# Kernel optimization log

Measured on AMD Instinct MI355X. Metric: run time of the kernel, lower is better.

Reference implementation:

```python
import jax, jax.numpy as jnp
import numpy as np
import itertools

DIM = 384
KEY_DIM = 32
NUM_HEADS = 8
ATTN_RATIO = 4
RESOLUTION = 7
D = ATTN_RATIO * KEY_DIM          # 128
DH = D * NUM_HEADS                # 1024
H_QKV = DH + 2 * KEY_DIM * NUM_HEADS  # 1536
B = 2048
N = RESOLUTION ** 2               # 49


def _build_bias_idxs():
    points = list(itertools.product(range(RESOLUTION), range(RESOLUTION)))
    attention_offsets = {}
    idxs = []
    for p1 in points:
        for p2 in points:
            offset = (abs(p1[0] - p2[0]), abs(p1[1] - p2[1]))
            if offset not in attention_offsets:
                attention_offsets[offset] = len(attention_offsets)
            idxs.append(attention_offsets[offset])
    return np.array(idxs, dtype=np.int32).reshape(N, N), len(attention_offsets)


def setup_inputs() -> dict:
    key = jax.random.key(0)
    ks = jax.random.split(key, 6)
    bias_idxs_np, n_offsets = _build_bias_idxs()  # n_offsets == 49 for resolution 7
    x = jax.random.normal(ks[0], (B, N, DIM), dtype=jnp.float32)
    qkv_w = jax.random.normal(ks[1], (H_QKV, DIM), dtype=jnp.float32) * (DIM ** -0.5)
    qkv_b = jnp.zeros((H_QKV,), dtype=jnp.float32)
    proj_w = jax.random.normal(ks[2], (DIM, DH), dtype=jnp.float32) * (DH ** -0.5)
    proj_b = jnp.zeros((DIM,), dtype=jnp.float32)
    attn_bias = jax.random.normal(ks[3], (NUM_HEADS, n_offsets), dtype=jnp.float32) * 0.02
    bias_idxs = jnp.asarray(bias_idxs_np)
    return {"x": x, "qkv_w": qkv_w, "qkv_b": qkv_b, "proj_w": proj_w,
            "proj_b": proj_b, "attn_bias": attn_bias, "bias_idxs": bias_idxs}


def reference(x, qkv_w, qkv_b, proj_w, proj_b, attn_bias, bias_idxs):
    Bb, Nn, _ = x.shape
    scale = KEY_DIM ** -0.5
    qkv = x @ qkv_w.T + qkv_b                       # [B, N, 1536]
    qkv = qkv.reshape(Bb, Nn, NUM_HEADS, KEY_DIM + KEY_DIM + D)
    q = qkv[..., :KEY_DIM]                          # [B, N, H, kd]
    k = qkv[..., KEY_DIM:2 * KEY_DIM]               # [B, N, H, kd]
    v = qkv[..., 2 * KEY_DIM:]                      # [B, N, H, d]
    bias = attn_bias[:, bias_idxs]                  # [H, N, N] gathered rel-pos bias
    attn = jnp.einsum('bnhk,bmhk->bhnm', q, k) * scale + bias
    attn = jax.nn.softmax(attn, axis=-1)
    out = jnp.einsum('bhnm,bmhd->bnhd', attn, v).reshape(Bb, Nn, DH)
    return out @ proj_w.T + proj_b                  # [B, N, dim]
```

## Files before the change

kernel.cpp:

```cpp
#include <hip/hip_runtime.h>
#include <cstddef>
#include <cstdint>

#define TOK    49
#define KD     32
#define NH     8
#define DHEAD  128
#define HQKV   1536
#define DHTOT  1024
#define DIMM   384

typedef unsigned short u16;
typedef float  f32x4  __attribute__((ext_vector_type(4)));
typedef __bf16 bf16x8 __attribute__((ext_vector_type(8)));

typedef const __attribute__((address_space(1))) void gas_void;
typedef __attribute__((address_space(3))) void las_void;

static __device__ __forceinline__ u16 f2bf(float f) {
    unsigned int u = __builtin_bit_cast(unsigned int, f);
    return (u16)((u + 0x7fffu + ((u >> 16) & 1u)) >> 16);
}

static __device__ __forceinline__ int swz(int row, int c) {
    return (row << 6) + ((((c >> 3) ^ (row & 7)) << 3) | (c & 7));
}

static __device__ __forceinline__ int swzV(int row, int c) {
    return (row << 6) + ((((c >> 3) ^ (row & 7) ^ ((row >> 3) & 7)) << 3) | (c & 7));
}

static __device__ __forceinline__ int xcd_chunk(int bid, int nwg) {
    const int xcd = bid & 7, slot = bid >> 3;
    const int q = nwg >> 3, r = nwg & 7;
    return (xcd < r ? xcd * (q + 1) : r * (q + 1) + (xcd - r) * q) + slot;
}

#define BAR() __builtin_amdgcn_s_barrier()
#define WAIT_VM6()  asm volatile("s_waitcnt vmcnt(6)"  ::: "memory")
#define WAIT_VM12() asm volatile("s_waitcnt vmcnt(12)" ::: "memory")
#define WAIT_VM0()  asm volatile("s_waitcnt vmcnt(0)"  ::: "memory")
#define LGKM0_BAR() do { asm volatile("s_waitcnt lgkmcnt(0)" ::: "memory"); \
                         __builtin_amdgcn_s_barrier(); } while (0)

__global__ __launch_bounds__(256)
void cast_swz(const float* __restrict__ in, u16* __restrict__ out, int K8, long nchunk)
{
    long i = (long)blockIdx.x * 256 + threadIdx.x;
    const long stride = (long)gridDim.x * 256;
    for (; i < nchunk; i += stride) {
        const long row = i / K8;
        const int  c8  = (int)(i - row * K8);
        const int  slot = c8 & 7, tpan = c8 >> 3;
        float4 v0 = reinterpret_cast<const float4*>(in)[i * 2];
        float4 v1 = reinterpret_cast<const float4*>(in)[i * 2 + 1];
        uint4 o;
        o.x = f2bf(v0.x) | ((unsigned)f2bf(v0.y) << 16);
        o.y = f2bf(v0.z) | ((unsigned)f2bf(v0.w) << 16);
        o.z = f2bf(v1.x) | ((unsigned)f2bf(v1.y) << 16);
        o.w = f2bf(v1.z) | ((unsigned)f2bf(v1.w) << 16);
        *reinterpret_cast<uint4*>(out + row * (long)K8 * 8 + tpan * 64 +
                                  ((slot ^ ((int)row & 7)) << 3)) = o;
    }
}

__global__ __launch_bounds__(256)
void bias_expand(const float* __restrict__ attn_bias, const int* __restrict__ idxs,
                 float* __restrict__ bias_full, int n_off)
{
    int i = blockIdx.x * 256 + threadIdx.x;
    if (i < NH * TOK * TOK) {
        int h = i / (TOK * TOK), s = i - h * (TOK * TOK);
        bias_full[i] = attn_bias[h * n_off + idxs[s]];
    }
}

static __device__ __forceinline__ int frag_off(int row, int ks8fg) {
    return (row << 6) + (((ks8fg ^ (row & 7)) << 3));
}

__global__ __launch_bounds__(256)
void gemm_qkv(const float* __restrict__ X,
              const u16* __restrict__ W,
              const float* __restrict__ bias,
              u16* __restrict__ qkvb, int M)
{
    const int K = DIMM;
    const int NB2 = HQKV / 256;
    const int nwg = (M / 64) * NB2;
    const int wgid = xcd_chunk(blockIdx.x, nwg);
    const int bm = (wgid / NB2) * 64;
    const int bn = (wgid % NB2) * 256;

    __shared__ u16 Alds[2][64 * 64];
    __shared__ u16 B0lds[2][128 * 64];
    __shared__ u16 B1lds[2][128 * 64];

    const int t    = threadIdx.x;
    const int lane = t & 63;
    const int wv   = t >> 6;
    const int lrow = lane >> 3;
    const int lcol = (lane & 7) * 8;
    const int frow = lane & 15;
    const int fg   = lane >> 4;

    const int ar0 = t >> 3,           as0 = t & 7;
    const int ar1 = (t + 256) >> 3,   as1 = t & 7;

    f32x4 acc0[4][2], acc1[4][2];
    #pragma unroll
    for (int mi = 0; mi < 4; ++mi)
        #pragma unroll
        for (int nc = 0; nc < 2; ++nc) { acc0[mi][nc] = (f32x4)0.0f; acc1[mi][nc] = (f32x4)0.0f; }

    uint4 rA[2][4];

    auto ISSUE = [&](int buf, int k0) {
        #pragma unroll
        for (int i = 0; i < 4; ++i) {
            const int c   = i * 4 + wv;
            const int row = c * 8 + lrow;
            __builtin_amdgcn_global_load_lds((gas_void*)(W + (size_t)(bn + row) * K + k0 + lcol),
                                             (las_void*)(&B0lds[buf][c * 512]), 16, 0, 0);
        }
        #pragma unroll
        for (int i = 0; i < 4; ++i) {
            const int c   = i * 4 + wv;
            const int row = c * 8 + lrow;
            __builtin_amdgcn_global_load_lds((gas_void*)(W + (size_t)(bn + 128 + row) * K + k0 + lcol),
                                             (las_void*)(&B1lds[buf][c * 512]), 16, 0, 0);
        }
        const float* a0 = X + (size_t)(bm + ar0) * K + k0 + as0 * 8;
        const float* a1 = X + (size_t)(bm + ar1) * K + k0 + as1 * 8;
        rA[buf][0] = *reinterpret_cast<const uint4*>(a0);
        rA[buf][1] = *reinterpret_cast<const uint4*>(a0 + 4);
        rA[buf][2] = *reinterpret_cast<const uint4*>(a1);
        rA[buf][3] = *reinterpret_cast<const uint4*>(a1 + 4);
    };

    auto WRITE = [&](int buf) {
        #pragma unroll
        for (int l = 0; l < 2; ++l) {
            const int row = l ? ar1 : ar0;
            const int sl  = l ? as1 : as0;
            const float4 f0 = __builtin_bit_cast(float4, rA[buf][l * 2]);
            const float4 f1 = __builtin_bit_cast(float4, rA[buf][l * 2 + 1]);
            uint4 o;
            o.x = f2bf(f0.x) | ((unsigned)f2bf(f0.y) << 16);
            o.y = f2bf(f0.z) | ((unsigned)f2bf(f0.w) << 16);
            o.z = f2bf(f1.x) | ((unsigned)f2bf(f1.y) << 16);
            o.w = f2bf(f1.z) | ((unsigned)f2bf(f1.w) << 16);
            *reinterpret_cast<uint4*>(&Alds[buf][(row << 6) + ((sl ^ (row & 7)) << 3)]) = o;
        }
    };

    ISSUE(0, 0);
    ISSUE(1, 64);

    const int NT = 6;
    for (int ts = 0; ts < NT; ++ts) {
        WRITE(ts & 1);
        WAIT_VM12();
        LGKM0_BAR();
        const u16* Ab  = Alds[ts & 1];
        const u16* B0b = B0lds[ts & 1];
        const u16* B1b = B1lds[ts & 1];
        #pragma unroll
        for (int ks = 0; ks < 2; ++ks) {
            const int sl = ks * 4 + fg;
            bf16x8 af[4], b0[2], b1[2];
            #pragma unroll
            for (int mi = 0; mi < 4; ++mi)
                af[mi] = *reinterpret_cast<const bf16x8*>(&Ab[frag_off(mi * 16 + frow, sl)]);
            #pragma unroll
            for (int nc = 0; nc < 2; ++nc) {
                b0[nc] = *reinterpret_cast<const bf16x8*>(&B0b[frag_off(wv * 32 + nc * 16 + frow, sl)]);
                b1[nc] = *reinterpret_cast<const bf16x8*>(&B1b[frag_off(wv * 32 + nc * 16 + frow, sl)]);
            }
            #pragma unroll
            for (int mi = 0; mi < 4; ++mi)
                #pragma unroll
                for (int nc = 0; nc < 2; ++nc) {
                    acc0[mi][nc] = __builtin_amdgcn_mfma_f32_16x16x32_bf16(af[mi], b0[nc], acc0[mi][nc], 0, 0, 0);
                    acc1[mi][nc] = __builtin_amdgcn_mfma_f32_16x16x32_bf16(af[mi], b1[nc], acc1[mi][nc], 0, 0, 0);
                }
        }
        BAR();
        if (ts < NT - 2) ISSUE(ts & 1, (ts + 2) * 64);
    }

    const int rbase = (lane >> 4) * 4;
    #pragma unroll
    for (int half = 0; half < 2; ++half) {
        #pragma unroll
        for (int nc = 0; nc < 2; ++nc) {
            const int col = bn + half * 128 + wv * 32 + nc * 16 + frow;
            const float bv = bias[col];
            #pragma unroll
            for (int mi = 0; mi < 4; ++mi) {
                #pragma unroll
                for (int j = 0; j < 4; ++j) {
                    const int row = bm + mi * 16 + rbase + j;
                    const float v = half ? acc1[mi][nc][j] : acc0[mi][nc][j];
                    qkvb[(size_t)row * HQKV + col] = f2bf(v + bv);
                }
            }
        }
    }
}

__global__ __launch_bounds__(256)
void gemm_bf16_nt(const u16* __restrict__ A, const u16* __restrict__ W,
                  const float* __restrict__ bias, float* __restrict__ C,
                  int M, int N, int K)
{
    const int NB = N / 128;
    const int nwg = (M / 64) * NB;
    const int wgid = xcd_chunk(blockIdx.x, nwg);
    const int bm = (wgid / NB) * 64;
    const int bn = (wgid % NB) * 128;

    __shared__ u16 Alds[2][64 * 64];
    __shared__ u16 Blds[2][128 * 64];

    const int t    = threadIdx.x;
    const int lane = t & 63;
    const int wv   = t >> 6;
    const int lrow = lane >> 3;
    const int lcol = (lane & 7) * 8;
    const int frow = lane & 15;
    const int fg   = lane >> 4;

    f32x4 acc[4][2];
    #pragma unroll
    for (int mi = 0; mi < 4; ++mi)
        #pragma unroll
        for (int nc = 0; nc < 2; ++nc) acc[mi][nc] = (f32x4)0.0f;

    auto STAGE = [&](int buf, int k0) {
        #pragma unroll
        for (int i = 0; i < 2; ++i) {
            const int c   = i * 4 + wv;
            const int row = c * 8 + lrow;
            __builtin_amdgcn_global_load_lds((gas_void*)(A + (size_t)(bm + row) * K + k0 + lcol),
                                             (las_void*)(&Alds[buf][c * 512]), 16, 0, 0);
        }
        #pragma unroll
        for (int i = 0; i < 4; ++i) {
            const int c   = i * 4 + wv;
            const int row = c * 8 + lrow;
            __builtin_amdgcn_global_load_lds((gas_void*)(W + (size_t)(bn + row) * K + k0 + lcol),
                                             (las_void*)(&Blds[buf][c * 512]), 16, 0, 0);
        }
    };

    const int NT = K / 64;
    STAGE(0, 0);
    STAGE(1, 64);

    for (int ts = 0; ts < NT; ++ts) {
        if (ts < NT - 1) { WAIT_VM6(); }
        else             { WAIT_VM0(); }
        BAR();
        const u16* Ab = Alds[ts & 1];
        const u16* Bb = Blds[ts & 1];
        #pragma unroll
        for (int ks = 0; ks < 2; ++ks) {
            const int sl = ks * 4 + fg;
            bf16x8 af[4], bf[2];
            #pragma unroll
            for (int mi = 0; mi < 4; ++mi)
                af[mi] = *reinterpret_cast<const bf16x8*>(&Ab[frag_off(mi * 16 + frow, sl)]);
            #pragma unroll
            for (int nc = 0; nc < 2; ++nc)
                bf[nc] = *reinterpret_cast<const bf16x8*>(&Bb[frag_off(wv * 32 + nc * 16 + frow, sl)]);
            #pragma unroll
            for (int mi = 0; mi < 4; ++mi)
                #pragma unroll
                for (int nc = 0; nc < 2; ++nc)
                    acc[mi][nc] = __builtin_amdgcn_mfma_f32_16x16x32_bf16(af[mi], bf[nc], acc[mi][nc], 0, 0, 0);
        }
        BAR();
        if (ts < NT - 2) STAGE(ts & 1, (ts + 2) * 64);
    }

    const int rbase = (lane >> 4) * 4;
    #pragma unroll
    for (int nc = 0; nc < 2; ++nc) {
        const int col = bn + wv * 32 + nc * 16 + frow;
        const float bv = bias[col];
        #pragma unroll
        for (int mi = 0; mi < 4; ++mi) {
            #pragma unroll
            for (int j = 0; j < 4; ++j) {
                const int row = bm + mi * 16 + rbase + j;
                C[(size_t)row * N + col] = acc[mi][nc][j] + bv;
            }
        }
    }
}

#define NCH 5
struct Regs { uint4 v[NCH]; };

static __device__ __forceinline__ void load_regs(Regs& r, const u16* __restrict__ base, int t)
{
    #pragma unroll
    for (int k = 0; k < NCH; ++k) {
        const int idx = t + k * 256;
        if (idx < TOK * 24) {
            const int n = idx / 24, c = idx - n * 24;
            r.v[k] = *reinterpret_cast<const uint4*>(base + (size_t)n * HQKV + c * 8);
        }
    }
}

static __device__ __forceinline__ void write_lds(const Regs& r, u16* __restrict__ QK,
                                                 u16* __restrict__ V, int t)
{
    #pragma unroll
    for (int k = 0; k < NCH; ++k) {
        const int idx = t + k * 256;
        if (idx < TOK * 24) {
            const int n = idx / 24, c24 = idx - n * 24;
            if (c24 < 8) {
                *reinterpret_cast<uint4*>(&QK[(n << 6) + ((c24 ^ (n & 7)) << 3)]) = r.v[k];
            } else {
                const int d0 = (c24 - 8) * 8;
                u16 vals[8];
                *reinterpret_cast<uint4*>(vals) = r.v[k];
                #pragma unroll
                for (int e = 0; e < 8; ++e)
                    V[swzV(d0 + e, n)] = vals[e];
            }
        }
    }
}

static __device__ __forceinline__ void attn_head(
    const u16* __restrict__ QK, const u16* __restrict__ V,
    float* __restrict__ S, u16* __restrict__ Ps,
    const float* __restrict__ bh_bias, u16* __restrict__ ab,
    int b, int h, int t)
{
    const int lane = t & 63;
    const int w    = t >> 6;
    const int fr   = lane & 15;
    const int fg   = lane >> 4;

    bf16x8 qf = *reinterpret_cast<const bf16x8*>(&QK[swz(16 * w + fr, fg * 8)]);
    f32x4 sacc[4];
    #pragma unroll
    for (int nj = 0; nj < 4; ++nj) {
        bf16x8 kf = *reinterpret_cast<const bf16x8*>(&QK[swz(16 * nj + fr, 32 + fg * 8)]);
        sacc[nj] = __builtin_amdgcn_mfma_f32_16x16x32_bf16(qf, kf, (f32x4)0.0f, 0, 0, 0);
    }

    const float scale = 0.17677669529663687f;
    #pragma unroll
    for (int nj = 0; nj < 4; ++nj) {
        #pragma unroll
        for (int j = 0; j < 4; ++j) {
            const int row = 16 * w + fg * 4 + j;
            const int col = 16 * nj + fr;
            const int rn = row < TOK ? row : TOK - 1;
            const int cm = col < TOK ? col : TOK - 1;
            S[row * 80 + col] = sacc[nj][j] * scale + bh_bias[rn * TOK + cm];
        }
    }
    LGKM0_BAR();

    {
        const int n = t >> 2, j = t & 3;
        const float* Sr = &S[n * 80];
        float v[16];
        #pragma unroll
        for (int e = 0; e < 8; ++e) v[e]     = Sr[8 * j + e];
        #pragma unroll
        for (int e = 0; e < 8; ++e) v[8 + e] = Sr[32 + 8 * j + e];

        float mx = -1e30f;
        #pragma unroll
        for (int e = 0; e < 8; ++e) mx = fmaxf(mx, v[e]);
        #pragma unroll
        for (int e = 0; e < 8; ++e)
            if (32 + 8 * j + e < TOK) mx = fmaxf(mx, v[8 + e]);
        mx = fmaxf(mx, __shfl_xor(mx, 1, 4));
        mx = fmaxf(mx, __shfl_xor(mx, 2, 4));

        float sum = 0.f;
        #pragma unroll
        for (int e = 0; e < 8; ++e) { v[e] = __expf(v[e] - mx); sum += v[e]; }
        #pragma unroll
        for (int e = 0; e < 8; ++e) {
            const float ev = (32 + 8 * j + e < TOK) ? __expf(v[8 + e] - mx) : 0.f;
            v[8 + e] = ev; sum += ev;
        }
        sum += __shfl_xor(sum, 1, 4);
        sum += __shfl_xor(sum, 2, 4);
        const float inv = 1.f / sum;

        uint4 o;
        o.x = f2bf(v[0] * inv)  | ((unsigned)f2bf(v[1] * inv)  << 16);
        o.y = f2bf(v[2] * inv)  | ((unsigned)f2bf(v[3] * inv)  << 16);
        o.z = f2bf(v[4] * inv)  | ((unsigned)f2bf(v[5] * inv)  << 16);
        o.w = f2bf(v[6] * inv)  | ((unsigned)f2bf(v[7] * inv)  << 16);
        *reinterpret_cast<uint4*>(&Ps[swz(n, 8 * j)]) = o;
        o.x = f2bf(v[8] * inv)  | ((unsigned)f2bf(v[9] * inv)  << 16);
        o.y = f2bf(v[10] * inv) | ((unsigned)f2bf(v[11] * inv) << 16);
        o.z = f2bf(v[12] * inv) | ((unsigned)f2bf(v[13] * inv) << 16);
        o.w = f2bf(v[14] * inv) | ((unsigned)f2bf(v[15] * inv) << 16);
        *reinterpret_cast<uint4*>(&Ps[swz(n, 32 + 8 * j)]) = o;
    }
    LGKM0_BAR();

    f32x4 oacc[8];
    #pragma unroll
    for (int nj = 0; nj < 8; ++nj) oacc[nj] = (f32x4)0.0f;
    #pragma unroll
    for (int ks = 0; ks < 2; ++ks) {
        bf16x8 pf = *reinterpret_cast<const bf16x8*>(&Ps[swz(16 * w + fr, ks * 32 + fg * 8)]);
        #pragma unroll
        for (int nj = 0; nj < 8; ++nj) {
            bf16x8 vf = *reinterpret_cast<const bf16x8*>(&V[swzV(16 * nj + fr, ks * 32 + fg * 8)]);
            oacc[nj] = __builtin_amdgcn_mfma_f32_16x16x32_bf16(pf, vf, oacc[nj], 0, 0, 0);
        }
    }

    #pragma unroll
    for (int nj = 0; nj < 8; ++nj) {
        const int d = 16 * nj + fr;
        const int c = h * DHEAD + d;
        const int tp = c >> 6, sl = (c >> 3) & 7, cc = c & 7;
        #pragma unroll
        for (int j = 0; j < 4; ++j) {
            const int n = 16 * w + fg * 4 + j;
            if (n < TOK) {
                const int gr = b * TOK + n;
                ab[(size_t)gr * DHTOT + (tp << 6) + (((sl ^ (gr & 7)) << 3) | cc)] = f2bf(oacc[nj][j]);
            }
        }
    }
}

__global__ __launch_bounds__(256)
void attn_mfma(const u16* __restrict__ qkvb,
               const float* __restrict__ bias_full,
               u16* __restrict__ ab)
{
    __shared__ __align__(16) u16  QKs[64 * 64];
    __shared__ __align__(16) u16  Vts[128 * 64];
    __shared__ __align__(16) float S[64 * 80];
    __shared__ __align__(16) u16  Ps[64 * 64];

    const int t = threadIdx.x;
    const int b = blockIdx.x;
    const u16* base = qkvb + (size_t)b * TOK * HQKV;

    if (t < 128 * 2) {
        const int row = t >> 1, sl = 6 + (t & 1);
        *reinterpret_cast<uint4*>(&Vts[(row << 6) +
            (((sl ^ (row & 7) ^ ((row >> 3) & 7)) & 7) << 3)]) = make_uint4(0, 0, 0, 0);
    }
    __syncthreads();

    for (int flat = t; flat < TOK * 24; flat += 256) {
        const int n = flat / 24, c24 = flat - n * 24;
        uint4 u = *reinterpret_cast<const uint4*>(base + (size_t)n * HQKV + c24 * 8);
        if (c24 < 8) {
            *reinterpret_cast<uint4*>(&QKs[(n << 6) + ((c24 ^ (n & 7)) << 3)]) = u;
        } else {
            const int d0 = (c24 - 8) * 8;
            u16 vals[8];
            *reinterpret_cast<uint4*>(vals) = u;
            #pragma unroll
            for (int e = 0; e < 8; ++e)
                Vts[swzV(d0 + e, n)] = vals[e];
        }
    }

    Regs r;
    #pragma unroll 1
    for (int i = 0; i < NH; ++i) {
        if (i > 0) write_lds(r, QKs, Vts, t);
        if (i < NH - 1) load_regs(r, base + (i + 1) * 192, t);
        LGKM0_BAR();
        attn_head(QKs, Vts, S, Ps, bias_full + i * (TOK * TOK), ab, b, i, t);
        LGKM0_BAR();
    }
}

extern "C" void kernel_launch(void* const* d_in, const int* in_sizes, int n_in,
                              void* d_out, int out_size, void* d_ws, size_t ws_size,
                              hipStream_t stream)
{
    const float* x         = (const float*)d_in[0];
    const float* qkv_w     = (const float*)d_in[1];
    const float* qkv_b     = (const float*)d_in[2];
    const float* proj_w    = (const float*)d_in[3];
    const float* proj_b    = (const float*)d_in[4];
    const float* attn_bias = (const float*)d_in[5];
    const int*   bias_idxs = (const int*)d_in[6];

    const int Mtot  = in_sizes[0] / DIMM;
    const int Btot  = Mtot / TOK;
    const int n_off = in_sizes[5] / NH;

    const size_t nWq = (size_t)HQKV * DIMM;
    const size_t nWp = (size_t)DIMM * DHTOT;
    float* bias_full = (float*)d_ws;
    u16*   wq        = (u16*)((char*)d_ws + 76832);
    u16*   wp        = wq + nWq;
    u16*   dyn       = wp + nWp;
    const size_t fixed_bytes = 76832 + (nWq + nWp) * sizeof(u16);
    const size_t per_batch = (size_t)TOK * (HQKV + DHTOT) * 2;

    if (ws_size <= fixed_bytes) return;
    long BcL = (long)((ws_size - fixed_bytes) / per_batch);
    int Bc = (int)((BcL / 128) * 128);
    if (Bc <= 0) return;
    if (Bc > Btot) Bc = Btot;

    cast_swz<<<dim3(288), 256, 0, stream>>>(qkv_w, wq, DIMM / 8, (long)HQKV * (DIMM / 8));
    cast_swz<<<dim3(192), 256, 0, stream>>>(proj_w, wp, DHTOT / 8, (long)DIMM * (DHTOT / 8));
    bias_expand<<<dim3((NH * TOK * TOK + 255) / 256), 256, 0, stream>>>(attn_bias, bias_idxs, bias_full, n_off);

    for (int b0 = 0; b0 < Btot; b0 += Bc) {
        const int bc = (b0 + Bc <= Btot) ? Bc : (Btot - b0);
        const int Mc = bc * TOK;

        u16* qkvb = dyn;
        u16* abb  = qkvb + (size_t)Bc * TOK * HQKV;

        const float* xc   = x + (size_t)b0 * TOK * DIMM;
        float*       outc = (float*)d_out + (size_t)b0 * TOK * DIMM;

        gemm_qkv<<<dim3((Mc / 64) * (HQKV / 256)), 256, 0, stream>>>(xc, wq, qkv_b, qkvb, Mc);

        attn_mfma<<<dim3(bc), 256, 0, stream>>>(qkvb, bias_full, abb);

        gemm_bf16_nt<<<dim3((Mc / 64) * (DIMM / 128)), 256, 0, stream>>>(abb, wp, proj_b, outc, Mc, DIMM, DHTOT);
    }
}
```

Before: 605.0 us.

## Compute softmax in MFMA registers with lane shuffles, drop LDS score buffer

Softmax is now computed directly on the MFMA accumulator fragments. Row max and sum are reduced with 16-lane xor shuffles, so scores are no longer written to a float LDS buffer and re-read by a different thread mapping. This removes the S shared array (about 20KB of LDS) and two block barriers per head; each wave writes only its own P rows and uses a wave-local fence before the PV MFMA. The exchange is more shuffle instructions and scalar 2-byte LDS stores for P instead of vectorized 16-byte stores. Lower LDS use may allow more resident blocks per CU.

```diff
diff --git a/kernel.cpp b/kernel.cpp
--- a/kernel.cpp
+++ b/kernel.cpp
@@ -42,6 +42,8 @@
 #define WAIT_VM0()  asm volatile("s_waitcnt vmcnt(0)"  ::: "memory")
 #define LGKM0_BAR() do { asm volatile("s_waitcnt lgkmcnt(0)" ::: "memory"); \
                          __builtin_amdgcn_s_barrier(); } while (0)
+#define LGKM0_FENCE() do { asm volatile("s_waitcnt lgkmcnt(0)" ::: "memory"); \
+                           __builtin_amdgcn_sched_barrier(0); } while (0)
 
 __global__ __launch_bounds__(256)
 void cast_swz(const float* __restrict__ in, u16* __restrict__ out, int K8, long nchunk)
@@ -339,7 +341,7 @@
 
 static __device__ __forceinline__ void attn_head(
     const u16* __restrict__ QK, const u16* __restrict__ V,
-    float* __restrict__ S, u16* __restrict__ Ps,
+    u16* __restrict__ Ps,
     const float* __restrict__ bh_bias, u16* __restrict__ ab,
     int b, int h, int t)
 {
@@ -357,62 +359,62 @@
     }
 
     const float scale = 0.17677669529663687f;
+    float val[4][4];
     #pragma unroll
     for (int nj = 0; nj < 4; ++nj) {
+        const int col = 16 * nj + fr;
+        const int cm  = col < TOK ? col : TOK - 1;
         #pragma unroll
         for (int j = 0; j < 4; ++j) {
             const int row = 16 * w + fg * 4 + j;
-            const int col = 16 * nj + fr;
-            const int rn = row < TOK ? row : TOK - 1;
-            const int cm = col < TOK ? col : TOK - 1;
-            S[row * 80 + col] = sacc[nj][j] * scale + bh_bias[rn * TOK + cm];
-        }
-    }
-    LGKM0_BAR();
-
-    {
-        const int n = t >> 2, j = t & 3;
-        const float* Sr = &S[n * 80];
-        float v[16];
-        #pragma unroll
-        for (int e = 0; e < 8; ++e) v[e]     = Sr[8 * j + e];
-        #pragma unroll
-        for (int e = 0; e < 8; ++e) v[8 + e] = Sr[32 + 8 * j + e];
-
-        float mx = -1e30f;
-        #pragma unroll
-        for (int e = 0; e < 8; ++e) mx = fmaxf(mx, v[e]);
-        #pragma unroll
-        for (int e = 0; e < 8; ++e)
-            if (32 + 8 * j + e < TOK) mx = fmaxf(mx, v[8 + e]);
-        mx = fmaxf(mx, __shfl_xor(mx, 1, 4));
-        mx = fmaxf(mx, __shfl_xor(mx, 2, 4));
-
-        float sum = 0.f;
-        #pragma unroll
-        for (int e = 0; e < 8; ++e) { v[e] = __expf(v[e] - mx); sum += v[e]; }
-        #pragma unroll
-        for (int e = 0; e < 8; ++e) {
-            const float ev = (32 + 8 * j + e < TOK) ? __expf(v[8 + e] - mx) : 0.f;
-            v[8 + e] = ev; sum += ev;
-        }
-        sum += __shfl_xor(sum, 1, 4);
-        sum += __shfl_xor(sum, 2, 4);
-        const float inv = 1.f / sum;
-
-        uint4 o;
-        o.x = f2bf(v[0] * inv)  | ((unsigned)f2bf(v[1] * inv)  << 16);
-        o.y = f2bf(v[2] * inv)  | ((unsigned)f2bf(v[3] * inv)  << 16);
-        o.z = f2bf(v[4] * inv)  | ((unsigned)f2bf(v[5] * inv)  << 16);
-        o.w = f2bf(v[6] * inv)  | ((unsigned)f2bf(v[7] * inv)  << 16);
-        *reinterpret_cast<uint4*>(&Ps[swz(n, 8 * j)]) = o;
-        o.x = f2bf(v[8] * inv)  | ((unsigned)f2bf(v[9] * inv)  << 16);
-        o.y = f2bf(v[10] * inv) | ((unsigned)f2bf(v[11] * inv) << 16);
-        o.z = f2bf(v[12] * inv) | ((unsigned)f2bf(v[13] * inv) << 16);
-        o.w = f2bf(v[14] * inv) | ((unsigned)f2bf(v[15] * inv) << 16);
-        *reinterpret_cast<uint4*>(&Ps[swz(n, 32 + 8 * j)]) = o;
-    }
-    LGKM0_BAR();
+            const int rn  = row < TOK ? row : TOK - 1;
+            val[nj][j] = (col < TOK)
+                ? sacc[nj][j] * scale + bh_bias[rn * TOK + cm]
+                : -1e30f;
+        }
+    }
+
+    float mx[4], sum[4];
+    #pragma unroll
+    for (int j = 0; j < 4; ++j)
+        mx[j] = fmaxf(fmaxf(val[0][j], val[1][j]), fmaxf(val[2][j], val[3][j]));
+    #pragma unroll
+    for (int m = 1; m <= 8; m <<= 1)
+        #pragma unroll
+        for (int j = 0; j < 4; ++j)
+            mx[j] = fmaxf(mx[j], __shfl_xor(mx[j], m));
+
+    float ex[4][4];
+    #pragma unroll
+    for (int j = 0; j < 4; ++j) sum[j] = 0.f;
+    #pragma unroll
+    for (int nj = 0; nj < 4; ++nj) {
+        const int col = 16 * nj + fr;
+        #pragma unroll
+        for (int j = 0; j < 4; ++j) {
+            const float e = (col < TOK) ? __expf(val[nj][j] - mx[j]) : 0.f;
+            ex[nj][j] = e;
+            sum[j] += e;
+        }
+    }
+    #pragma unroll
+    for (int m = 1; m <= 8; m <<= 1)
+        #pragma unroll
+        for (int j = 0; j < 4; ++j)
+            sum[j] += __shfl_xor(sum[j], m);
+
+    float inv[4];
+    #pragma unroll
+    for (int j = 0; j < 4; ++j) inv[j] = 1.f / sum[j];
+
+    #pragma unroll
+    for (int nj = 0; nj < 4; ++nj) {
+        #pragma unroll
+        for (int j = 0; j < 4; ++j) {
+            Ps[swz(16 * w + fg * 4 + j, 16 * nj + fr)] = f2bf(ex[nj][j] * inv[j]);
+        }
+    }
+    LGKM0_FENCE();
 
     f32x4 oacc[8];
     #pragma unroll
@@ -448,10 +450,9 @@
                const float* __restrict__ bias_full,
                u16* __restrict__ ab)
 {
-    __shared__ __align__(16) u16  QKs[64 * 64];
-    __shared__ __align__(16) u16  Vts[128 * 64];
-    __shared__ __align__(16) float S[64 * 80];
-    __shared__ __align__(16) u16  Ps[64 * 64];
+    __shared__ __align__(16) u16 QKs[64 * 64];
+    __shared__ __align__(16) u16 Vts[128 * 64];
+    __shared__ __align__(16) u16 Ps[64 * 64];
 
     const int t = threadIdx.x;
     const int b = blockIdx.x;
@@ -485,7 +486,7 @@
         if (i > 0) write_lds(r, QKs, Vts, t);
         if (i < NH - 1) load_regs(r, base + (i + 1) * 192, t);
         LGKM0_BAR();
-        attn_head(QKs, Vts, S, Ps, bias_full + i * (TOK * TOK), ab, b, i, t);
+        attn_head(QKs, Vts, Ps, bias_full + i * (TOK * TOK), ab, b, i, t);
         LGKM0_BAR();
     }
 }
```

Result: slower. 708.0 us (+17.0%).
